# Performance work log

Measured on AMD Instinct MI355X. Metric: run time of the kernel, lower is better.

## Reference

```python
import jax, jax.numpy as jnp
import numpy as np

V, D, H, O = 32000, 256, 512, 6
B, T = 128, 2048


def setup_inputs() -> dict:
    key = jax.random.key(0)
    ks = jax.random.split(key, 8)
    s = lambda k, shp, fan: jax.random.normal(k, shp, jnp.float32) / np.float32(np.sqrt(fan))
    return dict(
        token_ids=jax.random.randint(ks[0], (B, T), 0, V),
        emb=s(ks[1], (V, D), D),
        gru_wih=s(ks[2], (3 * H, D), D),
        gru_whh=s(ks[3], (3 * H, H), H),
        gru_b=jnp.zeros((3 * H,), jnp.float32),
        gru_bn=jnp.zeros((H,), jnp.float32),
        lstm_wih=s(ks[4], (4 * H, H), H),
        lstm_whh=s(ks[5], (4 * H, H), H),
        lstm_b=jnp.zeros((4 * H,), jnp.float32),
        head_w=s(ks[6], (O, H), H),
        head_b=jnp.zeros((O,), jnp.float32),
    )


def reference(token_ids, emb, gru_wih, gru_whh, gru_b, gru_bn,
              lstm_wih, lstm_whh, lstm_b, head_w, head_b):
    x = emb[token_ids]                      # (B, T, D) embedding lookup
    xs = jnp.swapaxes(x, 0, 1)              # (T, B, D) for scan over time
    h = gru_whh.shape[1]
    h0 = jnp.zeros((x.shape[0], h), x.dtype)

    def step(carry, xt):
        hg, hl, cl = carry
        # --- equinox GRUCell ---
        ig = xt @ gru_wih.T + gru_b         # (B, 3H)
        hh = hg @ gru_whh.T                 # (B, 3H)
        ir, iz, inn = jnp.split(ig, 3, axis=-1)
        hr, hz, hn = jnp.split(hh, 3, axis=-1)
        r = jax.nn.sigmoid(ir + hr)
        z = jax.nn.sigmoid(iz + hz)
        n = jnp.tanh(inn + r * (hn + gru_bn))
        hg_new = n + z * (hg - n)           # == (1-z)*n + z*hg
        # --- equinox LSTMCell (input = GRU output) ---
        lin = hg_new @ lstm_wih.T + hl @ lstm_whh.T + lstm_b  # (B, 4H)
        i_, f_, g_, o_ = jnp.split(lin, 4, axis=-1)
        c_new = jax.nn.sigmoid(f_) * cl + jax.nn.sigmoid(i_) * jnp.tanh(g_)
        h_new = jax.nn.sigmoid(o_) * jnp.tanh(c_new)
        return (hg_new, h_new, c_new), None

    (_, h_final, _), _ = jax.lax.scan(step, (h0, h0, h0), xs)
    return h_final @ head_w.T + head_b      # (B, O)
```

## Files before the change

### kernel.cpp

```cpp
#include <hip/hip_runtime.h>
#include <hip/hip_bf16.h>


typedef short v8s __attribute__((ext_vector_type(8)));
typedef float v4f __attribute__((ext_vector_type(4)));
typedef unsigned long long u64;

#define T_STEPS 2048
#define RING_OFF 8192
#define DYN_LDS 150816

#define MFMA16(a, b, c) __builtin_amdgcn_mfma_f32_16x16x32_bf16((a), (b), (c), 0, 0, 0)

__device__ __forceinline__ v4f v4zero() { v4f z = {0.f, 0.f, 0.f, 0.f}; return z; }
__device__ __forceinline__ float sigf(float x) { return 1.f / (1.f + __expf(-x)); }
__device__ __forceinline__ float tanhf_fast(float x) { return 1.f - 2.f / (1.f + __expf(2.f * x)); }

__device__ __forceinline__ ushort f2us(float v) {
  __hip_bfloat16 b = __float2bfloat16(v);
  return *reinterpret_cast<ushort*>(&b);
}
__device__ __forceinline__ float us2f(ushort u) {
  __hip_bfloat16 b;
  *reinterpret_cast<ushort*>(&b) = u;
  return __bfloat162float(b);
}
__device__ __forceinline__ void cvt_hilo(float v, ushort& h, ushort& l) {
  __hip_bfloat16 bh = __float2bfloat16(v);
  float r = v - __bfloat162float(bh);
  __hip_bfloat16 bl = __float2bfloat16(r);
  h = *reinterpret_cast<ushort*>(&bh);
  l = *reinterpret_cast<ushort*>(&bl);
}
__device__ __forceinline__ void stage4(ushort* hi, ushort* lo, const float* src) {
  float4 v = *(const float4*)src;
  float a[4] = {v.x, v.y, v.z, v.w};
#pragma unroll
  for (int j = 0; j < 4; ++j) { ushort h, l; cvt_hilo(a[j], h, l); hi[j] = h; lo[j] = l; }
}
__device__ __forceinline__ void stage4h(ushort* hi, const float* src) {
  float4 v = *(const float4*)src;
  float a[4] = {v.x, v.y, v.z, v.w};
#pragma unroll
  for (int j = 0; j < 4; ++j) hi[j] = f2us(a[j]);
}
__device__ __forceinline__ void st_wt(ushort* p, ushort v) {
  __hip_atomic_store(p, v, __ATOMIC_RELAXED, __HIP_MEMORY_SCOPE_AGENT);
}
__device__ __forceinline__ void st_row32(ushort* rowp, int r16, ushort uh) {
  unsigned v32 = (unsigned)uh;
  unsigned nb = (unsigned)__shfl_xor((int)v32, 1);
  if (!(r16 & 1)) v32 |= (nb << 16);
  unsigned hi32 = (unsigned)__shfl_xor((int)v32, 2);
  if ((r16 & 3) == 0) {
    u64 v = (u64)v32 | ((u64)hi32 << 32);
    __hip_atomic_store((u64*)(rowp + r16), v, __ATOMIC_RELAXED, __HIP_MEMORY_SCOPE_AGENT);
  }
}
__device__ __forceinline__ v8s ld_a16(const ushort* p) {
  u64 a = __hip_atomic_load((const u64*)p, __ATOMIC_RELAXED, __HIP_MEMORY_SCOPE_AGENT);
  u64 b = __hip_atomic_load((const u64*)p + 1, __ATOMIC_RELAXED, __HIP_MEMORY_SCOPE_AGENT);
  union { u64 u[2]; v8s v; } r;
  r.u[0] = a; r.u[1] = b;
  return r.v;
}

__device__ __forceinline__ int poll_ge(const int* p, int tgt, long& budget) {
  while (budget > 0) {
    if (__hip_atomic_load(p, __ATOMIC_RELAXED, __HIP_MEMORY_SCOPE_AGENT) >= tgt) return 1;
    __builtin_amdgcn_s_sleep(1);
    --budget;
  }
  return 0;
}
__device__ __forceinline__ int pollep(const int* gepo, int ta,
                                      const int* lepo, int tb,
                                      int lane, long& budget, int& slack) {
  const int* p = (lane < 32) ? (gepo + lane) : (lepo + (lane - 32));
  const int t = (lane < 32) ? ta : tb;
  while (budget > 0) {
    int v = __hip_atomic_load(p, __ATOMIC_RELAXED, __HIP_MEMORY_SCOPE_AGENT);
    int d = v - t;
    if (__all(d >= 0)) {
      int m = d;
#pragma unroll
      for (int off = 1; off < 64; off <<= 1) {
        int o = __shfl_xor(m, off);
        m = (o < m) ? o : m;
      }
      slack = m;
      return 1;
    }
    __builtin_amdgcn_s_sleep(1);
    --budget;
  }
  return 0;
}

__global__ void __launch_bounds__(256, 1) rnn_persistent(
    const int* __restrict__ tok,
    const float* __restrict__ emb,
    const float* __restrict__ gwih,
    const float* __restrict__ gwhh,
    const float* __restrict__ gb,
    const float* __restrict__ gbn,
    const float* __restrict__ lwih,
    const float* __restrict__ lwhh,
    const float* __restrict__ lb,
    char* __restrict__ ws,
    int hstride, int has_lo, int rdm)
{
  extern __shared__ char smem[];
  const int tid  = threadIdx.x;
  const int wgid = blockIdx.x;
  const bool is_gru = (wgid < 64);
  const int sub = is_gru ? wgid : (wgid - 64);
  const int bg  = sub & 1;
  const int cg  = sub >> 1;
  const int colbase = cg * 16;
  const int b0 = bg * 64;
  const int lane = tid & 63;
  const int wave = tid >> 6;
  const int quad = lane >> 4;
  const int r16  = lane & 15;

  int* cnt = (int*)ws;
  int* gru_ep  = cnt + bg * 32;
  int* lstm_ep = cnt + 64 + bg * 32;
  int* boot    = cnt + 128;
  ushort* ring = (ushort*)(ws + RING_OFF);
  const int slotE = 128 * hstride;
  ushort* hlb = ring + (rdm + 1) * slotE;

  const int mrow  = wave * 16 + r16;
  const int bglob = b0 + wave * 16 + quad * 4;
  const int col   = colbase + r16;
  long budget = 3000000;
  int slack = 0;

  if (is_gru) {
    ushort* smemU = (ushort*)smem;
    const int WIH_HI = 0, WIH_LO = 12672, WHH_HI = 25344, WHH_LO = 50304;
    int* okf = (int*)(smem + 150528);

    for (int i = tid; i < 48 * 64; i += 256) {
      int row = i >> 6, q = (i & 63) * 4;
      int gate = row >> 4, c = colbase + (row & 15);
      stage4(&smemU[WIH_HI + row * 264 + q], &smemU[WIH_LO + row * 264 + q],
             gwih + (long)(gate * 512 + c) * 256 + q);
    }
    for (int i = tid; i < 48 * 128; i += 256) {
      int row = i >> 7, k = (i & 127) * 4;
      int gate = row >> 4, c = colbase + (row & 15);
      stage4(&smemU[WHH_HI + row * 520 + k], &smemU[WHH_LO + row * 520 + k],
             gwhh + (long)(gate * 512 + c) * 512 + k);
    }
    const float b_r  = gb[col];
    const float b_z  = gb[512 + col];
    const float b_in = gb[1024 + col];
    const float bnv  = gbn[col];
    __syncthreads();

    if (tid == 0) {
      __hip_atomic_fetch_add(boot, 1, __ATOMIC_RELEASE, __HIP_MEMORY_SCOPE_AGENT);
      long bb = 3000000;
      okf[0] = poll_ge(boot, 128, bb);
    }
    __syncthreads();
    if (!okf[0]) { if (wgid == 0 && tid == 0) st_wt(&hlb[slotE + 0], f2us(1.0e4f)); return; }

    v4f acc_r, acc_z, acc_nx;
    float hgreg[4] = {0.f, 0.f, 0.f, 0.f};
    float4 xa[16];

    auto prefetch_x = [&](int tn) {
      int ntok = tok[(b0 + mrow) * T_STEPS + tn];
      const float* xrow = emb + (long)ntok * 256;
#pragma unroll
      for (int kk = 0; kk < 8; ++kk) {
        xa[2 * kk]     = *(const float4*)(xrow + kk * 32 + quad * 8);
        xa[2 * kk + 1] = *(const float4*)(xrow + kk * 32 + quad * 8 + 4);
      }
    };
    auto accx_compute = [&]() {
      acc_r = v4zero(); acc_z = v4zero(); acc_nx = v4zero();
#pragma unroll
      for (int kk = 0; kk < 8; ++kk) {
        float xv[8] = {xa[2 * kk].x, xa[2 * kk].y, xa[2 * kk].z, xa[2 * kk].w,
                       xa[2 * kk + 1].x, xa[2 * kk + 1].y, xa[2 * kk + 1].z, xa[2 * kk + 1].w};
        v8s ahi, alo;
#pragma unroll
        for (int j = 0; j < 8; ++j) { ushort h, l; cvt_hilo(xv[j], h, l); ahi[j] = (short)h; alo[j] = (short)l; }
        const int orr = (r16) * 264 + kk * 32 + quad * 8;
        const int oz  = (16 + r16) * 264 + kk * 32 + quad * 8;
        const int on  = (32 + r16) * 264 + kk * 32 + quad * 8;
        v8s brh = *(const v8s*)&smemU[WIH_HI + orr], brl = *(const v8s*)&smemU[WIH_LO + orr];
        v8s bzh = *(const v8s*)&smemU[WIH_HI + oz],  bzl = *(const v8s*)&smemU[WIH_LO + oz];
        v8s bnh = *(const v8s*)&smemU[WIH_HI + on],  bnl = *(const v8s*)&smemU[WIH_LO + on];
        acc_r = MFMA16(ahi, brh, acc_r); acc_r = MFMA16(alo, brh, acc_r); acc_r = MFMA16(ahi, brl, acc_r);
        acc_z = MFMA16(ahi, bzh, acc_z); acc_z = MFMA16(alo, bzh, acc_z); acc_z = MFMA16(ahi, bzl, acc_z);
        acc_nx = MFMA16(ahi, bnh, acc_nx); acc_nx = MFMA16(alo, bnh, acc_nx); acc_nx = MFMA16(ahi, bnl, acc_nx);
      }
    };

    prefetch_x(0);
    accx_compute();

    for (int t = 0; t < T_STEPS; ++t) {
      if (t + 1 < T_STEPS) prefetch_x(t + 1);

      if (t > 0) {
        if (wave == 0) {
          int ok = 1;
          if (slack > 0) { --slack; }
          else ok = pollep(gru_ep, t, lstm_ep, t - rdm, lane, budget, slack);
          if (lane == 0) okf[0] = ok;
        }
        __syncthreads();
        if (!okf[0]) { if (tid == 0) st_wt(&hlb[slotE + 2 + wgid], f2us(100.f)); break; }
      }

      v8s ahi[16], alo[16];
      if (t > 0) {
        const ushort* hrow = ring + ((t - 1) & rdm) * slotE + (b0 + mrow) * hstride;
#pragma unroll
        for (int kk = 0; kk < 16; ++kk) {
          ahi[kk] = ld_a16(&hrow[kk * 32 + quad * 8]);
          if (has_lo) alo[kk] = ld_a16(&hrow[512 + kk * 32 + quad * 8]);
        }
      }

      v4f acc_nh = v4zero();
      if (t > 0) {
#pragma unroll
        for (int kk = 0; kk < 16; ++kk) {
          const int orr = (r16) * 520 + kk * 32 + quad * 8;
          const int oz  = (16 + r16) * 520 + kk * 32 + quad * 8;
          const int on  = (32 + r16) * 520 + kk * 32 + quad * 8;
          v8s brh = *(const v8s*)&smemU[WHH_HI + orr], brl = *(const v8s*)&smemU[WHH_LO + orr];
          v8s bzh = *(const v8s*)&smemU[WHH_HI + oz],  bzl = *(const v8s*)&smemU[WHH_LO + oz];
          v8s bnh = *(const v8s*)&smemU[WHH_HI + on],  bnl = *(const v8s*)&smemU[WHH_LO + on];
          acc_r = MFMA16(ahi[kk], brh, acc_r); acc_r = MFMA16(ahi[kk], brl, acc_r);
          acc_z = MFMA16(ahi[kk], bzh, acc_z); acc_z = MFMA16(ahi[kk], bzl, acc_z);
          acc_nh = MFMA16(ahi[kk], bnh, acc_nh); acc_nh = MFMA16(ahi[kk], bnl, acc_nh);
          if (has_lo) {
            acc_r = MFMA16(alo[kk], brh, acc_r);
            acc_z = MFMA16(alo[kk], bzh, acc_z);
            acc_nh = MFMA16(alo[kk], bnh, acc_nh);
          }
        }
      }

      ushort* slotT = ring + (t & rdm) * slotE;
#pragma unroll
      for (int rg = 0; rg < 4; ++rg) {
        float r = sigf(acc_r[rg] + b_r);
        float z = sigf(acc_z[rg] + b_z);
        float nn = tanhf_fast(acc_nx[rg] + b_in + r * (acc_nh[rg] + bnv));
        float hnew = nn + z * (hgreg[rg] - nn);
        hgreg[rg] = hnew;
        ushort uh = f2us(hnew);
        ushort* rp = &slotT[(bglob + rg) * hstride + colbase];
        st_row32(rp, r16, uh);
        if (has_lo) st_row32(rp + 512, r16, f2us(hnew - us2f(uh)));
      }

      __syncthreads();
      if (tid == 0)
        __hip_atomic_store(gru_ep + cg, t + 1, __ATOMIC_RELEASE, __HIP_MEMORY_SCOPE_AGENT);
      if (t + 1 < T_STEPS) accx_compute();
    }
  } else {
    ushort* smemU = (ushort*)smem;
    int* okf = (int*)(smem + 132096);

    for (int i = tid; i < 64 * 256; i += 256) {
      int row = i >> 8, k = (i & 255) * 4;
      int gate = row >> 4, c = colbase + (row & 15);
      long grow = gate * 512 + c;
      const float* src = (k < 512) ? (lwih + grow * 512 + k) : (lwhh + grow * 512 + (k - 512));
      stage4h(&smemU[row * 1032 + k], src);
    }
    const float b_i = lb[col];
    const float b_f = lb[512 + col];
    const float b_g = lb[1024 + col];
    const float b_o = lb[1536 + col];
    __syncthreads();

    if (tid == 0) {
      __hip_atomic_fetch_add(boot, 1, __ATOMIC_RELEASE, __HIP_MEMORY_SCOPE_AGENT);
      long bb = 3000000;
      okf[0] = poll_ge(boot, 128, bb);
    }
    __syncthreads();
    if (!okf[0]) { if (wgid == 64 && tid == 0) st_wt(&hlb[slotE + 1], f2us(1.0e4f)); return; }

    float creg[4] = {0.f, 0.f, 0.f, 0.f};

    for (int t = 0; t < T_STEPS; ++t) {
      if (wave == 0) {
        int ok = 1;
        if (slack > 0) { --slack; }
        else ok = pollep(gru_ep, t + 1, lstm_ep, t, lane, budget, slack);
        if (lane == 0) okf[0] = ok;
      }
      __syncthreads();
      if (!okf[0]) { if (tid == 0) st_wt(&hlb[slotE + 2 + wgid], f2us(100.f)); break; }

      v8s ghi[16], glo[16];
      {
        const ushort* hrow = ring + (t & rdm) * slotE + (b0 + mrow) * hstride;
#pragma unroll
        for (int kk = 0; kk < 16; ++kk) {
          ghi[kk] = ld_a16(&hrow[kk * 32 + quad * 8]);
          if (has_lo) glo[kk] = ld_a16(&hrow[512 + kk * 32 + quad * 8]);
        }
      }
      v8s lhi[16], llo[16];
      const ushort* lrow = hlb + ((t - 1) & 1) * slotE + (b0 + mrow) * hstride;
      if (t > 0) {
#pragma unroll
        for (int kk = 0; kk < 16; ++kk) lhi[kk] = ld_a16(&lrow[kk * 32 + quad * 8]);
      }

      v4f ai = v4zero(), af = v4zero(), ag = v4zero(), ao = v4zero();
#pragma unroll
      for (int kk = 0; kk < 16; ++kk) {
        v8s bi = *(const v8s*)&smemU[(r16) * 1032 + kk * 32 + quad * 8];
        v8s bf = *(const v8s*)&smemU[(16 + r16) * 1032 + kk * 32 + quad * 8];
        v8s bgv = *(const v8s*)&smemU[(32 + r16) * 1032 + kk * 32 + quad * 8];
        v8s bo = *(const v8s*)&smemU[(48 + r16) * 1032 + kk * 32 + quad * 8];
        ai = MFMA16(ghi[kk], bi, ai); af = MFMA16(ghi[kk], bf, af);
        ag = MFMA16(ghi[kk], bgv, ag); ao = MFMA16(ghi[kk], bo, ao);
        if (has_lo) {
          ai = MFMA16(glo[kk], bi, ai); af = MFMA16(glo[kk], bf, af);
          ag = MFMA16(glo[kk], bgv, ag); ao = MFMA16(glo[kk], bo, ao);
        }
      }

      if (t > 0) {
        if (has_lo) {
#pragma unroll
          for (int kk = 0; kk < 16; ++kk) llo[kk] = ld_a16(&lrow[512 + kk * 32 + quad * 8]);
        }
#pragma unroll
        for (int kk = 0; kk < 16; ++kk) {
          v8s bi = *(const v8s*)&smemU[(r16) * 1032 + 512 + kk * 32 + quad * 8];
          v8s bf = *(const v8s*)&smemU[(16 + r16) * 1032 + 512 + kk * 32 + quad * 8];
          v8s bgv = *(const v8s*)&smemU[(32 + r16) * 1032 + 512 + kk * 32 + quad * 8];
          v8s bo = *(const v8s*)&smemU[(48 + r16) * 1032 + 512 + kk * 32 + quad * 8];
          ai = MFMA16(lhi[kk], bi, ai); af = MFMA16(lhi[kk], bf, af);
          ag = MFMA16(lhi[kk], bgv, ag); ao = MFMA16(lhi[kk], bo, ao);
        }
        if (has_lo) {
#pragma unroll
          for (int kk = 0; kk < 16; ++kk) {
            v8s bi = *(const v8s*)&smemU[(r16) * 1032 + 512 + kk * 32 + quad * 8];
            v8s bf = *(const v8s*)&smemU[(16 + r16) * 1032 + 512 + kk * 32 + quad * 8];
            v8s bgv = *(const v8s*)&smemU[(32 + r16) * 1032 + 512 + kk * 32 + quad * 8];
            v8s bo = *(const v8s*)&smemU[(48 + r16) * 1032 + 512 + kk * 32 + quad * 8];
            ai = MFMA16(llo[kk], bi, ai); af = MFMA16(llo[kk], bf, af);
            ag = MFMA16(llo[kk], bgv, ag); ao = MFMA16(llo[kk], bo, ao);
          }
        }
      }

      ushort* hout = hlb + (t & 1) * slotE;
#pragma unroll
      for (int rg = 0; rg < 4; ++rg) {
        float i_ = sigf(ai[rg] + b_i), f_ = sigf(af[rg] + b_f);
        float g_ = tanhf_fast(ag[rg] + b_g), o_ = sigf(ao[rg] + b_o);
        float cn = f_ * creg[rg] + i_ * g_;
        creg[rg] = cn;
        float hv = o_ * tanhf_fast(cn);
        ushort uh = f2us(hv);
        ushort* rp = &hout[(bglob + rg) * hstride + colbase];
        st_row32(rp, r16, uh);
        if (has_lo) st_row32(rp + 512, r16, f2us(hv - us2f(uh)));
      }

      __syncthreads();
      if (tid == 0)
        __hip_atomic_store(lstm_ep + cg, t + 1, __ATOMIC_RELEASE, __HIP_MEMORY_SCOPE_AGENT);
    }
  }
}

__global__ void head_kernel(const char* __restrict__ ws,
                            const float* __restrict__ hw,
                            const float* __restrict__ hbias,
                            float* __restrict__ out,
                            int hstride, int has_lo, int rd) {
  const ushort* h1 = (const ushort*)(ws + RING_OFF) + (rd + 1) * 128 * hstride;
  const int b = blockIdx.x, l = threadIdx.x;
  const int k0 = l * 8;
  v8s hi = ld_a16(&h1[b * hstride + k0]);
  v8s lo;
  if (has_lo) lo = ld_a16(&h1[b * hstride + 512 + k0]);
  float acc[6] = {0.f, 0.f, 0.f, 0.f, 0.f, 0.f};
#pragma unroll
  for (int j = 0; j < 8; ++j) {
    float h = us2f((ushort)hi[j]);
    if (has_lo) h += us2f((ushort)lo[j]);
#pragma unroll
    for (int o = 0; o < 6; ++o) acc[o] += h * hw[o * 512 + k0 + j];
  }
#pragma unroll
  for (int o = 0; o < 6; ++o) {
    float v = acc[o];
    for (int off = 32; off > 0; off >>= 1) v += __shfl_down(v, off);
    if (l == 0) out[b * 6 + o] = v + hbias[o];
  }
}

__global__ void init_ws(int* cnt) {
  int i = blockIdx.x * blockDim.x + threadIdx.x;
  if (i < 2048)
    __hip_atomic_store(cnt + i, 0, __ATOMIC_RELAXED, __HIP_MEMORY_SCOPE_AGENT);
}

__global__ void ws_too_small_marker(float* out) {
  if (threadIdx.x == 0 && blockIdx.x == 0) out[0] = 12345.0f;
}

extern "C" void kernel_launch(void* const* d_in, const int* in_sizes, int n_in,
                              void* d_out, int out_size, void* d_ws, size_t ws_size,
                              hipStream_t stream) {
  const int*   tok  = (const int*)d_in[0];
  const float* emb  = (const float*)d_in[1];
  const float* gwih = (const float*)d_in[2];
  const float* gwhh = (const float*)d_in[3];
  const float* gb   = (const float*)d_in[4];
  const float* gbn  = (const float*)d_in[5];
  const float* lwih = (const float*)d_in[6];
  const float* lwhh = (const float*)d_in[7];
  const float* lb   = (const float*)d_in[8];
  const float* hw   = (const float*)d_in[9];
  const float* hb   = (const float*)d_in[10];

  (void)in_sizes; (void)n_in; (void)out_size;

  const size_t WS_D = (size_t)RING_OFF + 6ull * 128 * 1024 * 2;
  const size_t WS_A = (size_t)RING_OFF + 4ull * 128 * 1024 * 2;
  const size_t WS_B = (size_t)RING_OFF + 4ull * 128 * 512 * 2;
  if (ws_size < WS_B) {
    hipLaunchKernelGGL(ws_too_small_marker, dim3(1), dim3(64), 0, stream, (float*)d_out);
    return;
  }
  const int has_lo  = (ws_size >= (size_t)WS_A) ? 1 : 0;
  const int hstride = has_lo ? 1024 : 512;
  const int rd      = (ws_size >= (size_t)WS_D) ? 4 : 2;

  (void)hipFuncSetAttribute(reinterpret_cast<const void*>(rnn_persistent),
                            hipFuncAttributeMaxDynamicSharedMemorySize, DYN_LDS);
  hipLaunchKernelGGL(init_ws, dim3(8), dim3(256), 0, stream, (int*)d_ws);
  hipLaunchKernelGGL(rnn_persistent, dim3(128), dim3(256), DYN_LDS, stream,
                     tok, emb, gwih, gwhh, gb, gbn, lwih, lwhh, lb,
                     (char*)d_ws, hstride, has_lo, rd - 1);
  hipLaunchKernelGGL(head_kernel, dim3(128), dim3(64), 0, stream,
                     (const char*)d_ws, hw, hb, (float*)d_out, hstride, has_lo, rd);
}
```

Measured before the change: 36.88 ms.

## Place GRU/LSTM workgroups per XCD and use L2-local flags for same-die sync

Launches 256 workgroups and keeps half of them, mapping each role and batch group to a nominal XCD slot (wgid&7), so that workgroups sharing a batch group are expected to sit on the same die. At startup each workgroup records its hardware XCC id in a table. If placement is confirmed and the L2 writeback builtin exists, same-XCD producers and consumers exchange hidden states and epoch flags through non-coherent volatile stores and sc0 loads that stay in the local L2. Cross-die dependencies go through separate flags published after an L2 writeback. A per-launch salt on the epoch counters avoids stale flags. The aim is lower per-step synchronization latency in the 2048-step recurrence, at the cost of complexity and reliance on the hardware dispatch pattern and on cache-coherence assumptions.

```diff
diff --git a/kernel.cpp b/kernel.cpp
--- a/kernel.cpp
+++ b/kernel.cpp
@@ -9,6 +9,16 @@
 #define T_STEPS 2048
 #define RING_OFF 8192
 #define DYN_LDS 150816
+
+#if __has_builtin(__builtin_amdgcn_buffer_wbl2)
+#define HAS_WBL2 1
+#define WBL2() __builtin_amdgcn_buffer_wbl2()
+#else
+#define HAS_WBL2 0
+#define WBL2()
+#endif
+
+#define XCC_HWREG (20 | (0 << 6) | (3 << 11))
 
 #define MFMA16(a, b, c) __builtin_amdgcn_mfma_f32_16x16x32_bf16((a), (b), (c), 0, 0, 0)
 
@@ -47,14 +57,15 @@
 __device__ __forceinline__ void st_wt(ushort* p, ushort v) {
   __hip_atomic_store(p, v, __ATOMIC_RELAXED, __HIP_MEMORY_SCOPE_AGENT);
 }
-__device__ __forceinline__ void st_row32(ushort* rowp, int r16, ushort uh) {
+__device__ __forceinline__ void st_row32_m(ushort* rowp, int r16, ushort uh, int loc) {
   unsigned v32 = (unsigned)uh;
   unsigned nb = (unsigned)__shfl_xor((int)v32, 1);
   if (!(r16 & 1)) v32 |= (nb << 16);
   unsigned hi32 = (unsigned)__shfl_xor((int)v32, 2);
   if ((r16 & 3) == 0) {
     u64 v = (u64)v32 | ((u64)hi32 << 32);
-    __hip_atomic_store((u64*)(rowp + r16), v, __ATOMIC_RELAXED, __HIP_MEMORY_SCOPE_AGENT);
+    if (loc) *(volatile u64*)(rowp + r16) = v;
+    else __hip_atomic_store((u64*)(rowp + r16), v, __ATOMIC_RELAXED, __HIP_MEMORY_SCOPE_AGENT);
   }
 }
 __device__ __forceinline__ v8s ld_a16(const ushort* p) {
@@ -64,6 +75,12 @@
   r.u[0] = a; r.u[1] = b;
   return r.v;
 }
+__device__ __forceinline__ int ld_sc0(const int* p) {
+  int v;
+  asm volatile("global_load_dword %0, %1, off sc0\n\ts_waitcnt vmcnt(0)"
+               : "=v"(v) : "v"(p) : "memory");
+  return v;
+}
 
 __device__ __forceinline__ int poll_ge(const int* p, int tgt, long& budget) {
   while (budget > 0) {
@@ -73,13 +90,16 @@
   }
   return 0;
 }
-__device__ __forceinline__ int pollep(const int* gepo, int ta,
-                                      const int* lepo, int tb,
-                                      int lane, long& budget, int& slack) {
-  const int* p = (lane < 32) ? (gepo + lane) : (lepo + (lane - 32));
+__device__ __forceinline__ int pollmix(const int* lineA, int ta, int locA,
+                                       const int* lineB, int tb, int locB,
+                                       int lane, long& budget, int& slack) {
+  const int* p = (lane < 32) ? (lineA + lane) : (lineB + (lane - 32));
   const int t = (lane < 32) ? ta : tb;
+  const int sm = (lane < 32) ? locA : locB;
   while (budget > 0) {
-    int v = __hip_atomic_load(p, __ATOMIC_RELAXED, __HIP_MEMORY_SCOPE_AGENT);
+    int v;
+    if (sm) v = ld_sc0(p);
+    else v = __hip_atomic_load(p, __ATOMIC_RELAXED, __HIP_MEMORY_SCOPE_AGENT);
     int d = v - t;
     if (__all(d >= 0)) {
       int m = d;
@@ -113,10 +133,11 @@
   extern __shared__ char smem[];
   const int tid  = threadIdx.x;
   const int wgid = blockIdx.x;
-  const bool is_gru = (wgid < 64);
-  const int sub = is_gru ? wgid : (wgid - 64);
-  const int bg  = sub & 1;
-  const int cg  = sub >> 1;
+  const int xnom = wgid & 7;
+  if (xnom >= 4) return;
+  const bool is_gru = (xnom < 2);
+  const int bg  = xnom & 1;
+  const int cg  = wgid >> 3;
   const int colbase = cg * 16;
   const int b0 = bg * 64;
   const int lane = tid & 63;
@@ -125,9 +146,12 @@
   const int r16  = lane & 15;
 
   int* cnt = (int*)ws;
-  int* gru_ep  = cnt + bg * 32;
-  int* lstm_ep = cnt + 64 + bg * 32;
-  int* boot    = cnt + 128;
+  int* tab      = cnt + 64;
+  int* boot     = cnt + 320;
+  int* gloc_ep  = cnt + 384 + bg * 32;
+  int* lloc_ep  = cnt + 448 + bg * 32;
+  int* gllc_ep  = cnt + 512 + bg * 32;
+  int* lllc_ep  = cnt + 576 + bg * 32;
   ushort* ring = (ushort*)(ws + RING_OFF);
   const int slotE = 128 * hstride;
   ushort* hlb = ring + (rdm + 1) * slotE;
@@ -138,6 +162,8 @@
   long budget = 3000000;
   int slack = 0;
 
+  const int myxcd = (int)__builtin_amdgcn_s_getreg(XCC_HWREG);
+
   if (is_gru) {
     ushort* smemU = (ushort*)smem;
     const int WIH_HI = 0, WIH_LO = 12672, WHH_HI = 25344, WHH_LO = 50304;
@@ -162,12 +188,36 @@
     __syncthreads();
 
     if (tid == 0) {
+      int lid = __hip_atomic_load(cnt, __ATOMIC_RELAXED, __HIP_MEMORY_SCOPE_AGENT);
+      int salt = (lid & 0x3FFFF) << 12;
+      okf[1] = salt;
+      __hip_atomic_store(tab + wgid, myxcd + 1, __ATOMIC_RELAXED, __HIP_MEMORY_SCOPE_AGENT);
+      __hip_atomic_store(gloc_ep + cg, salt, __ATOMIC_RELAXED, __HIP_MEMORY_SCOPE_AGENT);
+      __hip_atomic_store(gllc_ep + cg, salt, __ATOMIC_RELAXED, __HIP_MEMORY_SCOPE_AGENT);
       __hip_atomic_fetch_add(boot, 1, __ATOMIC_RELEASE, __HIP_MEMORY_SCOPE_AGENT);
       long bb = 3000000;
       okf[0] = poll_ge(boot, 128, bb);
     }
     __syncthreads();
     if (!okf[0]) { if (wgid == 0 && tid == 0) st_wt(&hlb[slotE + 0], f2us(1.0e4f)); return; }
+    const int SALT = okf[1];
+
+    if (wave == 0) {
+      int i = lane & 31, g = lane >> 5;
+      int e0 = __hip_atomic_load(tab + 8 * i + g,     __ATOMIC_RELAXED, __HIP_MEMORY_SCOPE_AGENT);
+      int e1 = __hip_atomic_load(tab + 8 * i + g + 2, __ATOMIC_RELAXED, __HIP_MEMORY_SCOPE_AGENT);
+      u64 b0m = __ballot(e0 == __shfl(e0, (lane < 32) ? 0 : 32));
+      u64 b1m = __ballot(e1 == __shfl(e1, (lane < 32) ? 0 : 32));
+      int eq[4] = { (int)((b0m & 0xFFFFFFFFull) == 0xFFFFFFFFull),
+                    (int)((b0m >> 32) == 0xFFFFFFFFull),
+                    (int)((b1m & 0xFFFFFFFFull) == 0xFFFFFFFFull),
+                    (int)((b1m >> 32) == 0xFFFFFFFFull) };
+      int r0 = __shfl(e0, 0), r1 = __shfl(e0, 32), r2 = __shfl(e1, 0), r3 = __shfl(e1, 32);
+      int dist = (r0 != r1) && (r0 != r2) && (r0 != r3) && (r1 != r2) && (r1 != r3) && (r2 != r3);
+      if (lane == 0) okf[2] = eq[xnom] && dist && HAS_WBL2;
+    }
+    __syncthreads();
+    const int loc = okf[2];
 
     v4f acc_r, acc_z, acc_nx;
     float hgreg[4] = {0.f, 0.f, 0.f, 0.f};
@@ -213,7 +263,8 @@
         if (wave == 0) {
           int ok = 1;
           if (slack > 0) { --slack; }
-          else ok = pollep(gru_ep, t, lstm_ep, t - rdm, lane, budget, slack);
+          else ok = pollmix(gloc_ep, SALT + t, loc,
+                            lllc_ep, SALT + t - rdm, 0, lane, budget, slack);
           if (lane == 0) okf[0] = ok;
         }
         __syncthreads();
@@ -261,15 +312,23 @@
         hgreg[rg] = hnew;
         ushort uh = f2us(hnew);
         ushort* rp = &slotT[(bglob + rg) * hstride + colbase];
-        st_row32(rp, r16, uh);
-        if (has_lo) st_row32(rp + 512, r16, f2us(hnew - us2f(uh)));
+        st_row32_m(rp, r16, uh, loc);
+        if (has_lo) st_row32_m(rp + 512, r16, f2us(hnew - us2f(uh)), loc);
       }
 
       __syncthreads();
-      if (tid == 0)
-        __hip_atomic_store(gru_ep + cg, t + 1, __ATOMIC_RELEASE, __HIP_MEMORY_SCOPE_AGENT);
+      if (tid == 0) {
+        if (loc) *(volatile int*)(gloc_ep + cg) = SALT + t + 1;
+        else __hip_atomic_store(gloc_ep + cg, SALT + t + 1, __ATOMIC_RELAXED, __HIP_MEMORY_SCOPE_AGENT);
+        if (loc) WBL2();
+      }
       if (t + 1 < T_STEPS) accx_compute();
-    }
+      if (tid == 0) {
+        if (loc) asm volatile("s_waitcnt vmcnt(0)" ::: "memory");
+        __hip_atomic_store(gllc_ep + cg, SALT + t + 1, __ATOMIC_RELAXED, __HIP_MEMORY_SCOPE_AGENT);
+      }
+    }
+    if (tid == 0 && HAS_WBL2) { WBL2(); asm volatile("s_waitcnt vmcnt(0)" ::: "memory"); }
   } else {
     ushort* smemU = (ushort*)smem;
     int* okf = (int*)(smem + 132096);
@@ -288,12 +347,36 @@
     __syncthreads();
 
     if (tid == 0) {
+      int lid = __hip_atomic_load(cnt, __ATOMIC_RELAXED, __HIP_MEMORY_SCOPE_AGENT);
+      int salt = (lid & 0x3FFFF) << 12;
+      okf[1] = salt;
+      __hip_atomic_store(tab + wgid, myxcd + 1, __ATOMIC_RELAXED, __HIP_MEMORY_SCOPE_AGENT);
+      __hip_atomic_store(lloc_ep + cg, salt, __ATOMIC_RELAXED, __HIP_MEMORY_SCOPE_AGENT);
+      __hip_atomic_store(lllc_ep + cg, salt, __ATOMIC_RELAXED, __HIP_MEMORY_SCOPE_AGENT);
       __hip_atomic_fetch_add(boot, 1, __ATOMIC_RELEASE, __HIP_MEMORY_SCOPE_AGENT);
       long bb = 3000000;
       okf[0] = poll_ge(boot, 128, bb);
     }
     __syncthreads();
-    if (!okf[0]) { if (wgid == 64 && tid == 0) st_wt(&hlb[slotE + 1], f2us(1.0e4f)); return; }
+    if (!okf[0]) { if (wgid == 2 && tid == 0) st_wt(&hlb[slotE + 1], f2us(1.0e4f)); return; }
+    const int SALT = okf[1];
+
+    if (wave == 0) {
+      int i = lane & 31, g = lane >> 5;
+      int e0 = __hip_atomic_load(tab + 8 * i + g,     __ATOMIC_RELAXED, __HIP_MEMORY_SCOPE_AGENT);
+      int e1 = __hip_atomic_load(tab + 8 * i + g + 2, __ATOMIC_RELAXED, __HIP_MEMORY_SCOPE_AGENT);
+      u64 b0m = __ballot(e0 == __shfl(e0, (lane < 32) ? 0 : 32));
+      u64 b1m = __ballot(e1 == __shfl(e1, (lane < 32) ? 0 : 32));
+      int eq[4] = { (int)((b0m & 0xFFFFFFFFull) == 0xFFFFFFFFull),
+                    (int)((b0m >> 32) == 0xFFFFFFFFull),
+                    (int)((b1m & 0xFFFFFFFFull) == 0xFFFFFFFFull),
+                    (int)((b1m >> 32) == 0xFFFFFFFFull) };
+      int r0 = __shfl(e0, 0), r1 = __shfl(e0, 32), r2 = __shfl(e1, 0), r3 = __shfl(e1, 32);
+      int dist = (r0 != r1) && (r0 != r2) && (r0 != r3) && (r1 != r2) && (r1 != r3) && (r2 != r3);
+      if (lane == 0) okf[2] = eq[xnom] && dist && HAS_WBL2;
+    }
+    __syncthreads();
+    const int loc = okf[2];
 
     float creg[4] = {0.f, 0.f, 0.f, 0.f};
 
@@ -301,7 +384,8 @@
       if (wave == 0) {
         int ok = 1;
         if (slack > 0) { --slack; }
-        else ok = pollep(gru_ep, t + 1, lstm_ep, t, lane, budget, slack);
+        else ok = pollmix(gllc_ep, SALT + t + 1, 0,
+                          lloc_ep, SALT + t, loc, lane, budget, slack);
         if (lane == 0) okf[0] = ok;
       }
       __syncthreads();
@@ -375,14 +459,18 @@
         float hv = o_ * tanhf_fast(cn);
         ushort uh = f2us(hv);
         ushort* rp = &hout[(bglob + rg) * hstride + colbase];
-        st_row32(rp, r16, uh);
-        if (has_lo) st_row32(rp + 512, r16, f2us(hv - us2f(uh)));
+        st_row32_m(rp, r16, uh, loc);
+        if (has_lo) st_row32_m(rp + 512, r16, f2us(hv - us2f(uh)), loc);
       }
 
       __syncthreads();
-      if (tid == 0)
-        __hip_atomic_store(lstm_ep + cg, t + 1, __ATOMIC_RELEASE, __HIP_MEMORY_SCOPE_AGENT);
-    }
+      if (tid == 0) {
+        if (loc) *(volatile int*)(lloc_ep + cg) = SALT + t + 1;
+        else __hip_atomic_store(lloc_ep + cg, SALT + t + 1, __ATOMIC_RELAXED, __HIP_MEMORY_SCOPE_AGENT);
+        __hip_atomic_store(lllc_ep + cg, SALT + t + 1, __ATOMIC_RELAXED, __HIP_MEMORY_SCOPE_AGENT);
+      }
+    }
+    if (tid == 0 && HAS_WBL2) { WBL2(); asm volatile("s_waitcnt vmcnt(0)" ::: "memory"); }
   }
 }
 
@@ -415,7 +503,9 @@
 
 __global__ void init_ws(int* cnt) {
   int i = blockIdx.x * blockDim.x + threadIdx.x;
-  if (i < 2048)
+  if (i == 0)
+    __hip_atomic_fetch_add(cnt, 1, __ATOMIC_RELAXED, __HIP_MEMORY_SCOPE_AGENT);
+  if (i >= 64 && i < 2048)
     __hip_atomic_store(cnt + i, 0, __ATOMIC_RELAXED, __HIP_MEMORY_SCOPE_AGENT);
 }
 
@@ -454,7 +544,7 @@
   (void)hipFuncSetAttribute(reinterpret_cast<const void*>(rnn_persistent),
                             hipFuncAttributeMaxDynamicSharedMemorySize, DYN_LDS);
   hipLaunchKernelGGL(init_ws, dim3(8), dim3(256), 0, stream, (int*)d_ws);
-  hipLaunchKernelGGL(rnn_persistent, dim3(128), dim3(256), DYN_LDS, stream,
+  hipLaunchKernelGGL(rnn_persistent, dim3(256), dim3(256), DYN_LDS, stream,
                      tok, emb, gwih, gwhh, gb, gbn, lwih, lwhh, lb,
                      (char*)d_ws, hstride, has_lo, rd - 1);
   hipLaunchKernelGGL(head_kernel, dim3(128), dim3(64), 0, stream,
```

Measured after the change: 38.46 ms. +4.3%, slower.
